# Optimization experiments

Hardware: AMD Instinct MI355X
Metric: run time of the kernel (lower is better)

## Reference

```python
import jax, jax.numpy as jnp
import numpy as np

B, S, E, H = 2, 2048, 1024, 16
D = E // H

def setup_inputs() -> dict:
    key = jax.random.key(0)
    ks = jax.random.split(key, 5)
    return {
        "hidden_states": jax.random.normal(ks[0], (B, S, E), dtype=jnp.float32),
        "c_attn_w": jax.random.normal(ks[1], (E, 3 * E), dtype=jnp.float32) * 0.02,
        "c_attn_b": jax.random.normal(ks[2], (3 * E,), dtype=jnp.float32) * 0.02,
        "c_proj_w": jax.random.normal(ks[3], (E, E), dtype=jnp.float32) * 0.02,
        "c_proj_b": jax.random.normal(ks[4], (E,), dtype=jnp.float32) * 0.02,
    }

def reference(hidden_states, c_attn_w, c_attn_b, c_proj_w, c_proj_b):
    x = hidden_states                      # [B, S, E]
    b, s, _ = x.shape
    w_q, w_k, w_v = jnp.split(c_attn_w, 3, axis=1)   # each [E, E]
    q_b, k_b, v_b = jnp.split(c_attn_b, 3, axis=0)   # each [E]

    # value projection
    v = x @ w_v + v_b                                        # [B,S,E]
    v = v.reshape(b, s, H, D).transpose(0, 2, 1, 3)          # [B,H,S,D]

    # fused query: ((x Wq + qb) Wk^T + kb)
    q = (x @ w_q + q_b) @ w_k.T + k_b                        # [B,S,E]
    qh = q.reshape(b, s, H, D).transpose(0, 2, 1, 3)         # [B,H,S,D]

    # key side is RAW hidden states split per head
    kh = x.reshape(b, s, H, D).transpose(0, 2, 1, 3)         # [B,H,S,D]

    scale = 1.0 / jnp.float32(D) ** 0.5
    scores = jnp.einsum("bhqd,bhkd->bhqk",
                        qh.astype(jnp.float32),
                        kh.astype(jnp.float32)) * scale       # [B,H,S,S] fp32

    causal = jnp.tril(jnp.ones((s, s), dtype=bool))
    mask_value = jnp.finfo(jnp.float32).min
    scores = jnp.where(causal[None, None], scores, mask_value)

    probs = jax.nn.softmax(scores, axis=-1).astype(v.dtype)  # [B,H,S,S]

    out = jnp.einsum("bhqk,bhkd->bhqd", probs, v)            # [B,H,S,D]
    out = out.transpose(0, 2, 1, 3).reshape(b, s, E)         # [B,S,E]
    out = out @ c_proj_w + c_proj_b
    return out
```

## Files before the change

### kernel.cpp

```cpp
#include <hip/hip_runtime.h>

typedef __attribute__((ext_vector_type(8))) __bf16 bf16x8;
typedef __attribute__((ext_vector_type(4))) __bf16 bf16x4;
typedef __attribute__((ext_vector_type(4))) float f32x4;

typedef __attribute__((address_space(1))) void as1_void;
typedef __attribute__((address_space(3))) void as3_void;

__device__ __forceinline__ void gl_lds16(const void* g, void* l) {
    __builtin_amdgcn_global_load_lds((const as1_void*)g, (as3_void*)l, 16, 0, 0);
}

__device__ __forceinline__ const bf16x8* swz(const __bf16* base, int row, int chunk) {
    return (const bf16x8*)((const char*)base + row * 128 + ((chunk ^ (row & 7)) * 16));
}

#define QSCALE (0.125f * 1.44269504f)

__global__ __launch_bounds__(256) void prep_kernel(
    const float* __restrict__ x, const float* __restrict__ caw,
    const float* __restrict__ cab, const float* __restrict__ cpw,
    __bf16* __restrict__ xb, __bf16* __restrict__ wvt,
    __bf16* __restrict__ wkn, __bf16* __restrict__ wqn,
    __bf16* __restrict__ wpt, float* __restrict__ bqv)
{
    __shared__ float tile[32 * 33];
    int bid = blockIdx.x;
    int tid = threadIdx.x;
    if (bid < 1024) {
        int nt = bid >> 5, kt = bid & 31;
        int tx = tid & 31, ty = tid >> 5;
        int n0 = nt * 32, k0 = kt * 32;
#pragma unroll
        for (int i = 0; i < 4; ++i)
            tile[(ty + i * 8) * 33 + tx] = caw[(long)(k0 + ty + i * 8) * 3072 + 2048 + n0 + tx];
        __syncthreads();
#pragma unroll
        for (int i = 0; i < 4; ++i)
            wvt[(long)(n0 + ty + i * 8) * 1024 + k0 + tx] = (__bf16)tile[tx * 33 + ty + i * 8];
    } else if (bid < 2048) {
        int v = bid - 1024;
        int nt = v >> 5, kt = v & 31;
        int tx = tid & 31, ty = tid >> 5;
        int n0 = nt * 32, k0 = kt * 32;
#pragma unroll
        for (int i = 0; i < 4; ++i)
            tile[(ty + i * 8) * 33 + tx] = cpw[(long)(k0 + ty + i * 8) * 1024 + n0 + tx];
        __syncthreads();
#pragma unroll
        for (int i = 0; i < 4; ++i)
            wpt[(long)(n0 + ty + i * 8) * 1024 + k0 + tx] = (__bf16)tile[tx * 33 + ty + i * 8];
    } else if (bid < 3072) {
        int e = (bid - 2048) * 1024 + tid * 4;
        int n = e >> 10, k = e & 1023;
        float4 f = *(const float4*)(caw + (long)n * 3072 + 1024 + k);
        bf16x4 o = {(__bf16)f.x, (__bf16)f.y, (__bf16)f.z, (__bf16)f.w};
        *(bf16x4*)(wkn + e) = o;
    } else if (bid < 4096) {
        int e = (bid - 3072) * 1024 + tid * 4;
        int n = e >> 10, k = e & 1023;
        float4 f = *(const float4*)(caw + (long)n * 3072 + k);
        bf16x4 o = {(__bf16)f.x, (__bf16)f.y, (__bf16)f.z, (__bf16)f.w};
        *(bf16x4*)(wqn + e) = o;
    } else if (bid < 8192) {
        long e = (long)(bid - 4096) * 1024 + tid * 4;
        float4 f = *(const float4*)(x + e);
        bf16x4 o = {(__bf16)f.x, (__bf16)f.y, (__bf16)f.z, (__bf16)f.w};
        *(bf16x4*)(xb + e) = o;
    } else {
        int k = bid - 8192;
        int wave = tid >> 6, lane = tid & 63;
        float qv[16];
#pragma unroll
        for (int u = 0; u < 4; ++u) {
            float4 q4 = *(const float4*)(cab + u * 256 + lane * 4);
            qv[u * 4 + 0] = q4.x; qv[u * 4 + 1] = q4.y;
            qv[u * 4 + 2] = q4.z; qv[u * 4 + 3] = q4.w;
        }
        for (int i = 0; i < 16; ++i) {
            int n = k * 64 + wave * 16 + i;
            float s = 0.f;
#pragma unroll
            for (int u = 0; u < 4; ++u) {
                float4 w4 = *(const float4*)(caw + (long)n * 3072 + 1024 + u * 256 + lane * 4);
                s += w4.x * qv[u * 4 + 0] + w4.y * qv[u * 4 + 1]
                   + w4.z * qv[u * 4 + 2] + w4.w * qv[u * 4 + 3];
            }
#pragma unroll
            for (int off = 1; off < 64; off <<= 1) s += __shfl_xor(s, off);
            if (lane == 0) bqv[n] = (s + cab[1024 + n]) * QSCALE;
        }
        if (tid < 64) bqv[1024 + k * 64 + tid] = cab[2048 + k * 64 + tid];
    }
}

template <bool BF16OUT, int BN>
__global__ __launch_bounds__(256) void gemm_bt(
    const __bf16* __restrict__ A, int lda,
    const __bf16* __restrict__ B, int ldb,
    const float* __restrict__ bias,
    void* __restrict__ C, int ldc, int K, float oscale)
{
    constexpr int NT = BN / 32;
    __shared__ __bf16 As[128 * 64];
    __shared__ __bf16 Bs[BN * 64];
    const int tid = threadIdx.x;
    const int lane = tid & 63;
    const int wave = tid >> 6;
    const int quad = lane >> 4, l16 = lane & 15;
    const long m0 = (long)blockIdx.y * 128;
    const long n0 = (long)blockIdx.x * BN;
    const int wm = (wave >> 1) * 64, wn = (wave & 1) * (BN / 2);

    f32x4 acc[4][NT] = {};

    for (int k0 = 0; k0 < K; k0 += 64) {
#pragma unroll
        for (int c = tid; c < (128 + BN) * 8; c += 256) {
            int row = c >> 3, cc = (c & 7) ^ (row & 7);
            if (row < 128)
                gl_lds16(A + (m0 + row) * lda + k0 + cc * 8, As + c * 8);
            else
                gl_lds16(B + (n0 + row - 128) * ldb + k0 + cc * 8, Bs + (c - 1024) * 8);
        }
        __syncthreads();
#pragma unroll
        for (int kk = 0; kk < 2; ++kk) {
            bf16x8 af[4], bfr[NT];
#pragma unroll
            for (int i = 0; i < 4; ++i)
                af[i] = *swz(As, wm + i * 16 + l16, kk * 4 + quad);
#pragma unroll
            for (int j = 0; j < NT; ++j)
                bfr[j] = *swz(Bs, wn + j * 16 + l16, kk * 4 + quad);
#pragma unroll
            for (int i = 0; i < 4; ++i)
#pragma unroll
                for (int j = 0; j < NT; ++j)
                    acc[i][j] = __builtin_amdgcn_mfma_f32_16x16x32_bf16(af[i], bfr[j], acc[i][j], 0, 0, 0);
        }
        __syncthreads();
    }
#pragma unroll
    for (int i = 0; i < 4; ++i) {
        long row = m0 + wm + i * 16 + quad * 4;
#pragma unroll
        for (int j = 0; j < NT; ++j) {
            int col = (int)n0 + wn + j * 16 + l16;
            float bb = bias ? bias[col] : 0.f;
#pragma unroll
            for (int r = 0; r < 4; ++r) {
                float v = (acc[i][j][r] + bb) * oscale;
                if (BF16OUT)
                    ((__bf16*)C)[(row + r) * ldc + col] = (__bf16)v;
                else
                    ((float*)C)[(row + r) * ldc + col] = v;
            }
        }
    }
}

__global__ __launch_bounds__(256) void gemm_qv(
    const __bf16* __restrict__ A,
    const __bf16* __restrict__ B,
    const float* __restrict__ bias,
    __bf16* __restrict__ Qout,
    __bf16* __restrict__ VTout)
{
    __shared__ __bf16 smem[128 * 136];
    __bf16* As = smem;
    __bf16* Bs = smem + 8192;
    const int tid = threadIdx.x;
    const int lane = tid & 63;
    const int wave = tid >> 6;
    const int quad = lane >> 4, l16 = lane & 15;
    const long m0 = (long)blockIdx.y * 128;
    const long n0 = (long)blockIdx.x * 128;
    const int wm = (wave >> 1) * 64, wn = (wave & 1) * 64;

    f32x4 acc[4][4] = {};

    for (int k0 = 0; k0 < 1024; k0 += 64) {
#pragma unroll
        for (int c = tid; c < 2048; c += 256) {
            int row = c >> 3, cc = (c & 7) ^ (row & 7);
            if (row < 128)
                gl_lds16(A + (m0 + row) * 1024 + k0 + cc * 8, As + c * 8);
            else
                gl_lds16(B + (n0 + row - 128) * 1024 + k0 + cc * 8, Bs + (c - 1024) * 8);
        }
        __syncthreads();
#pragma unroll
        for (int kk = 0; kk < 2; ++kk) {
            bf16x8 af[4], bfr[4];
#pragma unroll
            for (int i = 0; i < 4; ++i)
                af[i] = *swz(As, wm + i * 16 + l16, kk * 4 + quad);
#pragma unroll
            for (int j = 0; j < 4; ++j)
                bfr[j] = *swz(Bs, wn + j * 16 + l16, kk * 4 + quad);
#pragma unroll
            for (int i = 0; i < 4; ++i)
#pragma unroll
                for (int j = 0; j < 4; ++j)
                    acc[i][j] = __builtin_amdgcn_mfma_f32_16x16x32_bf16(af[i], bfr[j], acc[i][j], 0, 0, 0);
        }
        __syncthreads();
    }

    if (n0 < 1024) {
#pragma unroll
        for (int i = 0; i < 4; ++i) {
            long row = m0 + wm + i * 16 + quad * 4;
#pragma unroll
            for (int j = 0; j < 4; ++j) {
                int col = (int)n0 + wn + j * 16 + l16;
                float bb = bias[col];
#pragma unroll
                for (int r = 0; r < 4; ++r)
                    Qout[(row + r) * 1024 + col] = (__bf16)(acc[i][j][r] + bb);
            }
        }
    } else {
        __syncthreads();
#pragma unroll
        for (int i = 0; i < 4; ++i) {
#pragma unroll
            for (int j = 0; j < 4; ++j) {
                int col = (int)n0 + wn + j * 16 + l16;
                float bb = bias[col];
                bf16x4 v;
#pragma unroll
                for (int r = 0; r < 4; ++r) v[r] = (__bf16)(acc[i][j][r] + bb);
                *(bf16x4*)(smem + (wn + j * 16 + l16) * 136 + wm + i * 16 + quad * 4) = v;
            }
        }
        __syncthreads();
        const int d0 = (int)n0 - 1024;
        const int bb = (int)(m0 >> 11);
        const int sl = (int)(m0 & 2047);
#pragma unroll
        for (int pass = 0; pass < 16; ++pass) {
            int idx = pass * 256 + tid;
            int n = idx >> 5;
            int mc = (idx & 31) * 4;
            bf16x4 v = *(const bf16x4*)(smem + n * 136 + mc);
            *(bf16x4*)(VTout + ((long)(bb * 1024 + d0 + n)) * 2048 + sl + mc) = v;
        }
    }
}

__global__ __launch_bounds__(512) void attn_kernel(
    const __bf16* __restrict__ Q,
    const __bf16* __restrict__ Xb,
    const __bf16* __restrict__ VT,
    __bf16* __restrict__ O)
{
    __shared__ __bf16 Ks[2 * 8192];
    __shared__ __bf16 Vs[2 * 8192];
    __shared__ __bf16 Ps[8 * 1024];
    const int tid = threadIdx.x;
    const int lane = tid & 63;
    const int wave = tid >> 6;
    const int group = wave >> 2;
    const int w4 = wave & 3;
    const int quad = lane >> 4, l16 = lane & 15;
    const int qa = blockIdx.y;
    const int qb = 31 - qa;
    const int qt = group ? qb : qa;
    const int bh = blockIdx.x;
    const int b = bh >> 4, h = bh & 15;
    const long rowbase = (long)b * 2048;

    const int s0 = tid;
    const int c0 = ((s0 & 7) ^ ((s0 >> 3) & 7)) * 8;

    bf16x8 ones;
#pragma unroll
    for (int i = 0; i < 8; ++i) ones[i] = (__bf16)1.0f;

    bf16x8 qfr[2];
    {
        const __bf16* qp = Q + (rowbase + qt * 64 + w4 * 16 + l16) * 1024 + h * 64 + quad * 8;
        qfr[0] = *(const bf16x8*)(qp);
        qfr[1] = *(const bf16x8*)(qp + 32);
    }

    const __bf16* kp0 = Xb + (rowbase + (s0 >> 3)) * 1024 + h * 64 + c0;
    const __bf16* vp0 = VT + ((long)(b * 1024 + h * 64 + (s0 >> 3))) * 2048 + c0;

    auto stage_tile = [&](int j, int buf, int sub) {
        gl_lds16(kp0 + (long)j * 65536, Ks + buf * 8192 + sub * 4096 + s0 * 8);
        gl_lds16(vp0 + j * 64, Vs + buf * 8192 + sub * 4096 + s0 * 8);
    };
    stage_tile(0, 0, 0);
    stage_tile(1, 0, 1);

    const int nouter = (qb + 2) >> 1;

    f32x4 oacc[4] = {};
    f32x4 lacc = {};
    __bf16* Pw = Ps + wave * 1024;

    for (int jj = 0; jj < nouter; ++jj) {
        __syncthreads();
        if (jj + 1 < nouter) {
            stage_tile(2 * jj + 2, (jj + 1) & 1, 0);
            stage_tile(2 * jj + 3, (jj + 1) & 1, 1);
        }

#pragma unroll
        for (int sub = 0; sub < 2; ++sub) {
            const int j = 2 * jj + sub;
            if (j > qt) continue;
            const __bf16* Kb = Ks + (jj & 1) * 8192 + sub * 4096;
            const __bf16* Vb = Vs + (jj & 1) * 8192 + sub * 4096;

            bf16x8 kf[2][4], vf[2][4];
#pragma unroll
            for (int kk = 0; kk < 2; ++kk)
#pragma unroll
                for (int kt = 0; kt < 4; ++kt) {
                    kf[kk][kt] = *swz(Kb, kt * 16 + l16, kk * 4 + quad);
                    vf[kk][kt] = *swz(Vb, kt * 16 + l16, kk * 4 + quad);
                }

            f32x4 sacc[4] = {};
#pragma unroll
            for (int kk = 0; kk < 2; ++kk)
#pragma unroll
                for (int kt = 0; kt < 4; ++kt)
                    sacc[kt] = __builtin_amdgcn_mfma_f32_16x16x32_bf16(
                        kf[kk][kt], qfr[kk], sacc[kt], 0, 0, 0);

            if (j == qt) {
                const int qloc = w4 * 16 + l16;
#pragma unroll
                for (int kt = 0; kt < 4; ++kt) {
                    bf16x4 pk;
#pragma unroll
                    for (int r = 0; r < 4; ++r) {
                        float s = sacc[kt][r];
                        if (kt * 16 + quad * 4 + r > qloc) s = -1e30f;
                        pk[r] = (__bf16)exp2f(s);
                    }
                    *(bf16x4*)((char*)Pw + l16 * 128 +
                               (((kt * 2 + (quad >> 1)) ^ (l16 & 7)) * 16) + (quad & 1) * 8) = pk;
                }
            } else {
#pragma unroll
                for (int kt = 0; kt < 4; ++kt) {
                    bf16x4 pk;
#pragma unroll
                    for (int r = 0; r < 4; ++r)
                        pk[r] = (__bf16)exp2f(sacc[kt][r]);
                    *(bf16x4*)((char*)Pw + l16 * 128 +
                               (((kt * 2 + (quad >> 1)) ^ (l16 & 7)) * 16) + (quad & 1) * 8) = pk;
                }
            }

#pragma unroll
            for (int kk = 0; kk < 2; ++kk) {
                bf16x8 pf = *swz(Pw, l16, kk * 4 + quad);
                lacc = __builtin_amdgcn_mfma_f32_16x16x32_bf16(ones, pf, lacc, 0, 0, 0);
#pragma unroll
                for (int dt = 0; dt < 4; ++dt)
                    oacc[dt] = __builtin_amdgcn_mfma_f32_16x16x32_bf16(
                        vf[kk][dt], pf, oacc[dt], 0, 0, 0);
            }
        }
    }

    {
        float inv = 1.0f / lacc[0];
        long row = rowbase + qt * 64 + w4 * 16 + l16;
#pragma unroll
        for (int dt = 0; dt < 4; ++dt) {
            bf16x4 ov;
#pragma unroll
            for (int r = 0; r < 4; ++r) ov[r] = (__bf16)(oacc[dt][r] * inv);
            *(bf16x4*)(O + row * 1024 + h * 64 + dt * 16 + quad * 4) = ov;
        }
    }
}

extern "C" void kernel_launch(void* const* d_in, const int* in_sizes, int n_in,
                              void* d_out, int out_size, void* d_ws, size_t ws_size,
                              hipStream_t stream) {
    const float* x   = (const float*)d_in[0];
    const float* caw = (const float*)d_in[1];
    const float* cab = (const float*)d_in[2];
    const float* cpw = (const float*)d_in[3];
    const float* cpb = (const float*)d_in[4];

    char* p = (char*)d_ws;
    auto alloc = [&](size_t bytes) {
        void* r = (void*)p;
        p += (bytes + 255) & ~(size_t)255;
        return r;
    };
    __bf16* xb    = (__bf16*)alloc(4096UL * 1024 * 2);
    __bf16* mtb   = (__bf16*)alloc(1024UL * 1024 * 2);
    __bf16* wvt   = (__bf16*)alloc(1024UL * 1024 * 2);
    __bf16* wkn   = (__bf16*)alloc(1024UL * 1024 * 2);
    __bf16* wqn   = (__bf16*)alloc(1024UL * 1024 * 2);
    __bf16* wpt   = (__bf16*)alloc(1024UL * 1024 * 2);
    float*  bqv   = (float*) alloc(2048UL * 4);
    __bf16* qbuf  = (__bf16*)alloc(4096UL * 1024 * 2);
    __bf16* vt    = (__bf16*)alloc(2048UL * 2048 * 2);
    __bf16* attn  = (__bf16*)alloc(4096UL * 1024 * 2);

    prep_kernel<<<8208, 256, 0, stream>>>(x, caw, cab, cpw, xb, wvt, wkn, wqn, wpt, bqv);

    gemm_bt<true, 32><<<dim3(32, 8), 256, 0, stream>>>(wkn, 1024, wqn, 1024, nullptr,
                                                       (void*)mtb, 1024, 1024, QSCALE);
    gemm_qv<<<dim3(16, 32), 256, 0, stream>>>(xb, mtb, bqv, qbuf, vt);
    attn_kernel<<<dim3(32, 16), 512, 0, stream>>>(qbuf, xb, vt, attn);
    gemm_bt<false, 64><<<dim3(16, 32), 256, 0, stream>>>(attn, 1024, wpt, 1024, cpb,
                                                         d_out, 1024, 1024, 1.0f);
    (void)in_sizes; (void)n_in; (void)out_size; (void)ws_size;
}
```

Baseline: 183.4 us.

## Give each attention wave two query sub-tiles, halving block size to 256 threads

The attention kernel now runs 4 waves per block instead of 8. Each wave processes 32 query rows (two 16-row groups) and reuses each K/V fragment loaded from LDS for both groups. Each thread issues twice as many global-to-LDS loads per tile, and the P scratch per wave doubles. The aim is to halve the LDS fragment reads per MFMA. The cost is more accumulator registers per thread and fewer waves per block to hide latency, partly offset by launch_bounds(256,2).

```diff
diff --git a/kernel.cpp b/kernel.cpp
--- a/kernel.cpp
+++ b/kernel.cpp
@@ -250,7 +250,7 @@
     }
 }
 
-__global__ __launch_bounds__(512) void attn_kernel(
+__global__ __launch_bounds__(256, 2) void attn_kernel(
     const __bf16* __restrict__ Q,
     const __bf16* __restrict__ Xb,
     const __bf16* __restrict__ VT,
@@ -258,12 +258,12 @@
 {
     __shared__ __bf16 Ks[2 * 8192];
     __shared__ __bf16 Vs[2 * 8192];
-    __shared__ __bf16 Ps[8 * 1024];
+    __shared__ __bf16 Ps[4 * 2048];
     const int tid = threadIdx.x;
     const int lane = tid & 63;
     const int wave = tid >> 6;
-    const int group = wave >> 2;
-    const int w4 = wave & 3;
+    const int group = wave >> 1;
+    const int w2 = wave & 1;
     const int quad = lane >> 4, l16 = lane & 15;
     const int qa = blockIdx.y;
     const int qb = 31 - qa;
@@ -272,35 +272,43 @@
     const int b = bh >> 4, h = bh & 15;
     const long rowbase = (long)b * 2048;
 
-    const int s0 = tid;
-    const int c0 = ((s0 & 7) ^ ((s0 >> 3) & 7)) * 8;
+    const int i0 = tid, i1 = tid + 256;
+    const int r0 = i0 >> 3, c0 = ((i0 & 7) ^ (r0 & 7)) * 8;
+    const int r1 = i1 >> 3, c1 = ((i1 & 7) ^ (r1 & 7)) * 8;
 
     bf16x8 ones;
 #pragma unroll
     for (int i = 0; i < 8; ++i) ones[i] = (__bf16)1.0f;
 
-    bf16x8 qfr[2];
-    {
-        const __bf16* qp = Q + (rowbase + qt * 64 + w4 * 16 + l16) * 1024 + h * 64 + quad * 8;
-        qfr[0] = *(const bf16x8*)(qp);
-        qfr[1] = *(const bf16x8*)(qp + 32);
-    }
-
-    const __bf16* kp0 = Xb + (rowbase + (s0 >> 3)) * 1024 + h * 64 + c0;
-    const __bf16* vp0 = VT + ((long)(b * 1024 + h * 64 + (s0 >> 3))) * 2048 + c0;
+    bf16x8 qfr[2][2];
+#pragma unroll
+    for (int qg = 0; qg < 2; ++qg) {
+        const __bf16* qp = Q + (rowbase + qt * 64 + w2 * 32 + qg * 16 + l16) * 1024 + h * 64 + quad * 8;
+        qfr[qg][0] = *(const bf16x8*)(qp);
+        qfr[qg][1] = *(const bf16x8*)(qp + 32);
+    }
+
+    const __bf16* kp0 = Xb + (rowbase + r0) * 1024 + h * 64 + c0;
+    const __bf16* kp1 = Xb + (rowbase + r1) * 1024 + h * 64 + c1;
+    const __bf16* vp0 = VT + ((long)(b * 1024 + h * 64 + r0)) * 2048 + c0;
+    const __bf16* vp1 = VT + ((long)(b * 1024 + h * 64 + r1)) * 2048 + c1;
 
     auto stage_tile = [&](int j, int buf, int sub) {
-        gl_lds16(kp0 + (long)j * 65536, Ks + buf * 8192 + sub * 4096 + s0 * 8);
-        gl_lds16(vp0 + j * 64, Vs + buf * 8192 + sub * 4096 + s0 * 8);
+        __bf16* kd = Ks + buf * 8192 + sub * 4096;
+        __bf16* vd = Vs + buf * 8192 + sub * 4096;
+        gl_lds16(kp0 + (long)j * 65536, kd + i0 * 8);
+        gl_lds16(kp1 + (long)j * 65536, kd + i1 * 8);
+        gl_lds16(vp0 + j * 64, vd + i0 * 8);
+        gl_lds16(vp1 + j * 64, vd + i1 * 8);
     };
     stage_tile(0, 0, 0);
     stage_tile(1, 0, 1);
 
     const int nouter = (qb + 2) >> 1;
 
-    f32x4 oacc[4] = {};
-    f32x4 lacc = {};
-    __bf16* Pw = Ps + wave * 1024;
+    f32x4 oacc[4][2] = {};
+    f32x4 lacc[2] = {};
+    __bf16* Pw = Ps + wave * 2048;
 
     for (int jj = 0; jj < nouter; ++jj) {
         __syncthreads();
@@ -325,60 +333,73 @@
                     vf[kk][kt] = *swz(Vb, kt * 16 + l16, kk * 4 + quad);
                 }
 
-            f32x4 sacc[4] = {};
+            f32x4 sacc[4][2] = {};
 #pragma unroll
             for (int kk = 0; kk < 2; ++kk)
 #pragma unroll
                 for (int kt = 0; kt < 4; ++kt)
-                    sacc[kt] = __builtin_amdgcn_mfma_f32_16x16x32_bf16(
-                        kf[kk][kt], qfr[kk], sacc[kt], 0, 0, 0);
+#pragma unroll
+                    for (int qg = 0; qg < 2; ++qg)
+                        sacc[kt][qg] = __builtin_amdgcn_mfma_f32_16x16x32_bf16(
+                            kf[kk][kt], qfr[qg][kk], sacc[kt][qg], 0, 0, 0);
 
             if (j == qt) {
-                const int qloc = w4 * 16 + l16;
-#pragma unroll
-                for (int kt = 0; kt < 4; ++kt) {
-                    bf16x4 pk;
-#pragma unroll
-                    for (int r = 0; r < 4; ++r) {
-                        float s = sacc[kt][r];
-                        if (kt * 16 + quad * 4 + r > qloc) s = -1e30f;
-                        pk[r] = (__bf16)exp2f(s);
+#pragma unroll
+                for (int kt = 0; kt < 4; ++kt)
+#pragma unroll
+                    for (int qg = 0; qg < 2; ++qg) {
+                        const int qloc = w2 * 32 + qg * 16 + l16;
+                        bf16x4 pk;
+#pragma unroll
+                        for (int r = 0; r < 4; ++r) {
+                            float s = sacc[kt][qg][r];
+                            if (kt * 16 + quad * 4 + r > qloc) s = -1e30f;
+                            pk[r] = (__bf16)exp2f(s);
+                        }
+                        *(bf16x4*)((char*)Pw + (qg * 16 + l16) * 128 +
+                                   (((kt * 2 + (quad >> 1)) ^ (l16 & 7)) * 16) + (quad & 1) * 8) = pk;
                     }
-                    *(bf16x4*)((char*)Pw + l16 * 128 +
-                               (((kt * 2 + (quad >> 1)) ^ (l16 & 7)) * 16) + (quad & 1) * 8) = pk;
+            } else {
+#pragma unroll
+                for (int kt = 0; kt < 4; ++kt)
+#pragma unroll
+                    for (int qg = 0; qg < 2; ++qg) {
+                        bf16x4 pk;
+#pragma unroll
+                        for (int r = 0; r < 4; ++r)
+                            pk[r] = (__bf16)exp2f(sacc[kt][qg][r]);
+                        *(bf16x4*)((char*)Pw + (qg * 16 + l16) * 128 +
+                                   (((kt * 2 + (quad >> 1)) ^ (l16 & 7)) * 16) + (quad & 1) * 8) = pk;
+                    }
+            }
+
+#pragma unroll
+            for (int kk = 0; kk < 2; ++kk) {
+                bf16x8 pf[2];
+#pragma unroll
+                for (int qg = 0; qg < 2; ++qg) {
+                    pf[qg] = *swz(Pw, qg * 16 + l16, kk * 4 + quad);
+                    lacc[qg] = __builtin_amdgcn_mfma_f32_16x16x32_bf16(ones, pf[qg], lacc[qg], 0, 0, 0);
                 }
-            } else {
-#pragma unroll
-                for (int kt = 0; kt < 4; ++kt) {
-                    bf16x4 pk;
-#pragma unroll
-                    for (int r = 0; r < 4; ++r)
-                        pk[r] = (__bf16)exp2f(sacc[kt][r]);
-                    *(bf16x4*)((char*)Pw + l16 * 128 +
-                               (((kt * 2 + (quad >> 1)) ^ (l16 & 7)) * 16) + (quad & 1) * 8) = pk;
-                }
-            }
-
-#pragma unroll
-            for (int kk = 0; kk < 2; ++kk) {
-                bf16x8 pf = *swz(Pw, l16, kk * 4 + quad);
-                lacc = __builtin_amdgcn_mfma_f32_16x16x32_bf16(ones, pf, lacc, 0, 0, 0);
 #pragma unroll
                 for (int dt = 0; dt < 4; ++dt)
-                    oacc[dt] = __builtin_amdgcn_mfma_f32_16x16x32_bf16(
-                        vf[kk][dt], pf, oacc[dt], 0, 0, 0);
-            }
-        }
-    }
-
-    {
-        float inv = 1.0f / lacc[0];
-        long row = rowbase + qt * 64 + w4 * 16 + l16;
+#pragma unroll
+                    for (int qg = 0; qg < 2; ++qg)
+                        oacc[dt][qg] = __builtin_amdgcn_mfma_f32_16x16x32_bf16(
+                            vf[kk][dt], pf[qg], oacc[dt][qg], 0, 0, 0);
+            }
+        }
+    }
+
+#pragma unroll
+    for (int qg = 0; qg < 2; ++qg) {
+        float inv = 1.0f / lacc[qg][0];
+        long row = rowbase + qt * 64 + w2 * 32 + qg * 16 + l16;
 #pragma unroll
         for (int dt = 0; dt < 4; ++dt) {
             bf16x4 ov;
 #pragma unroll
-            for (int r = 0; r < 4; ++r) ov[r] = (__bf16)(oacc[dt][r] * inv);
+            for (int r = 0; r < 4; ++r) ov[r] = (__bf16)(oacc[dt][qg][r] * inv);
             *(bf16x4*)(O + row * 1024 + h * 64 + dt * 16 + quad * 4) = ov;
         }
     }
@@ -415,7 +436,7 @@
     gemm_bt<true, 32><<<dim3(32, 8), 256, 0, stream>>>(wkn, 1024, wqn, 1024, nullptr,
                                                        (void*)mtb, 1024, 1024, QSCALE);
     gemm_qv<<<dim3(16, 32), 256, 0, stream>>>(xb, mtb, bqv, qbuf, vt);
-    attn_kernel<<<dim3(32, 16), 512, 0, stream>>>(qbuf, xb, vt, attn);
+    attn_kernel<<<dim3(32, 16), 256, 0, stream>>>(qbuf, xb, vt, attn);
     gemm_bt<false, 64><<<dim3(16, 32), 256, 0, stream>>>(attn, 1024, wpt, 1024, cpb,
                                                          d_out, 1024, 1024, 1.0f);
     (void)in_sizes; (void)n_in; (void)out_size; (void)ws_size;
```

Result: slower. 191.8 us (+4.6%).
